# Kernel optimization log

Hardware: AMD Instinct MI355X
Metric: run time of the kernel (lower is better)

## Reference

```python
import jax, jax.numpy as jnp
import numpy as np
import math

N = 30000
E = 600000
IN_DIM = 256
HID = 64
EMB = 64
HEADS = 4
EPS = 1e-5


def _glorot(key, shape):
    fan_in, fan_out = shape[0], shape[1]
    lim = math.sqrt(6.0 / (fan_in + fan_out))
    return jax.random.uniform(key, shape, jnp.float32, -lim, lim)


def setup_inputs() -> dict:
    key = jax.random.key(0)
    ks = jax.random.split(key, 24)
    inp = {
        "x": jax.random.normal(ks[0], (N, IN_DIM), jnp.float32),
        "edge_index": jax.random.randint(ks[1], (2, E), 0, N, jnp.int64),
    }
    # layer 1: in=IN_DIM, out per head=HID, heads=HEADS -> width HID*HEADS
    w1 = HID * HEADS
    inp.update({
        "w1q": _glorot(ks[2], (IN_DIM, w1)), "b1q": jnp.zeros((w1,), jnp.float32),
        "w1k": _glorot(ks[3], (IN_DIM, w1)), "b1k": jnp.zeros((w1,), jnp.float32),
        "w1v": _glorot(ks[4], (IN_DIM, w1)), "b1v": jnp.zeros((w1,), jnp.float32),
        "w1s": _glorot(ks[5], (IN_DIM, w1)), "b1s": jnp.zeros((w1,), jnp.float32),
        "g1": jnp.ones((w1,), jnp.float32), "be1": jnp.zeros((w1,), jnp.float32),
    })
    # layer 2: in=HID*HEADS, out per head=EMB -> width EMB*HEADS
    w2 = EMB * HEADS
    inp.update({
        "w2q": _glorot(ks[6], (w1, w2)), "b2q": jnp.zeros((w2,), jnp.float32),
        "w2k": _glorot(ks[7], (w1, w2)), "b2k": jnp.zeros((w2,), jnp.float32),
        "w2v": _glorot(ks[8], (w1, w2)), "b2v": jnp.zeros((w2,), jnp.float32),
        "w2s": _glorot(ks[9], (w1, w2)), "b2s": jnp.zeros((w2,), jnp.float32),
        "g2": jnp.ones((w2,), jnp.float32), "be2": jnp.zeros((w2,), jnp.float32),
    })
    return inp


def transformer_conv(x, edge_index, wq, bq, wk, bk, wv, bv, ws, bs, heads, out_ch):
    n = x.shape[0]
    q = (x @ wq + bq).reshape(n, heads, out_ch)
    k = (x @ wk + bk).reshape(n, heads, out_ch)
    v = (x @ wv + bv).reshape(n, heads, out_ch)
    src, dst = edge_index[0], edge_index[1]
    # per-edge gather: [E, H, C]
    qi, kj, vj = q[dst], k[src], v[src]
    alpha = jnp.sum(qi * kj, axis=-1) / math.sqrt(out_ch)  # [E, H]
    # segment softmax over incoming edges of each target node
    amax = jax.lax.stop_gradient(jax.ops.segment_max(alpha, dst, num_segments=n))
    ex = jnp.exp(alpha - amax[dst])
    denom = jax.ops.segment_sum(ex, dst, num_segments=n)
    alpha = ex / denom[dst]
    # scatter-add weighted values back to targets
    out = jax.ops.segment_sum(vj * alpha[..., None], dst, num_segments=n)
    out = out.reshape(n, heads * out_ch)
    return out + x @ ws + bs  # root/skip connection


def batch_norm(x, gamma, beta):
    mean = jnp.mean(x, axis=0)
    var = jnp.mean(jnp.square(x - mean), axis=0)  # biased, training-mode BN
    return (x - mean) * jax.lax.rsqrt(var + EPS) * gamma + beta


def leaky_relu(x):
    return jnp.where(x >= 0, x, 0.1 * x)


def reference(x, edge_index, w1q, b1q, w1k, b1k, w1v, b1v, w1s, b1s, g1, be1,
              w2q, b2q, w2k, b2k, w2v, b2v, w2s, b2s, g2, be2):
    h = transformer_conv(x, edge_index, w1q, b1q, w1k, b1k, w1v, b1v, w1s, b1s, HEADS, HID)
    h = leaky_relu(batch_norm(h, g1, be1))
    h = transformer_conv(h, edge_index, w2q, b2q, w2k, b2k, w2v, b2v, w2s, b2s, HEADS, EMB)
    h = leaky_relu(batch_norm(h, g2, be2))
    return h
```

## Files before the change

kernel.cpp:

```cpp
#include <hip/hip_runtime.h>
#include <math.h>

#define NODES 30000
#define EDGES 600000
#define QKVS_W 1024
#define OUT_W 256
#define BN_EPS 1e-5f

typedef __attribute__((ext_vector_type(8))) __bf16 bf16x8;
typedef __attribute__((ext_vector_type(4))) float f32x4;

__device__ __forceinline__ unsigned short f2bf(float f) {
    union { float f; unsigned int u; } v; v.f = f;
    unsigned int r = v.u + 0x7FFFu + ((v.u >> 16) & 1u);
    return (unsigned short)(r >> 16);
}
__device__ __forceinline__ float bf2f(unsigned short u) {
    union { unsigned int u; float f; } v; v.u = ((unsigned int)u) << 16;
    return v.f;
}
__device__ __forceinline__ float bflo(unsigned int u) {
    union { unsigned int u; float f; } v; v.u = u << 16;
    return v.f;
}
__device__ __forceinline__ float bfhi(unsigned int u) {
    union { unsigned int u; float f; } v; v.u = u & 0xffff0000u;
    return v.f;
}

typedef const __attribute__((address_space(1))) void* gas_p;
typedef __attribute__((address_space(3))) void* las_p;
__device__ __forceinline__ void gload_lds16(const void* g, void* l) {
    __builtin_amdgcn_global_load_lds((gas_p)g, (las_p)l, 16, 0, 0);
}


__global__ __launch_bounds__(256) void k_count(const int* __restrict__ ei, int* __restrict__ deg) {
    int e = blockIdx.x * 256 + threadIdx.x;
    if (e < EDGES) atomicAdd(&deg[ei[EDGES + e]], 1);
}

__global__ __launch_bounds__(256) void k_blocksum(const int* __restrict__ deg, int* __restrict__ bsum) {
    __shared__ int sh[256];
    int i = blockIdx.x * 256 + threadIdx.x;
    sh[threadIdx.x] = (i < NODES) ? deg[i] : 0;
    __syncthreads();
    for (int off = 128; off > 0; off >>= 1) {
        if (threadIdx.x < off) sh[threadIdx.x] += sh[threadIdx.x + off];
        __syncthreads();
    }
    if (threadIdx.x == 0) bsum[blockIdx.x] = sh[0];
}

__global__ __launch_bounds__(128) void k_scanb(const int* __restrict__ bsum, int* __restrict__ bbase, int nb) {
    __shared__ int sh[128];
    int t = threadIdx.x;
    int v = (t < nb) ? bsum[t] : 0;
    sh[t] = v;
    __syncthreads();
    for (int off = 1; off < 128; off <<= 1) {
        int add = (t >= off) ? sh[t - off] : 0;
        __syncthreads();
        sh[t] += add;
        __syncthreads();
    }
    if (t < nb) bbase[t] = sh[t] - v;
}

__global__ __launch_bounds__(256) void k_localscan(const int* __restrict__ deg, const int* __restrict__ bbase,
                                                   int* __restrict__ rowptr, int* __restrict__ cursor) {
    __shared__ int sh[256];
    int i = blockIdx.x * 256 + threadIdx.x;
    int v = (i < NODES) ? deg[i] : 0;
    sh[threadIdx.x] = v;
    __syncthreads();
    for (int off = 1; off < 256; off <<= 1) {
        int add = (threadIdx.x >= off) ? sh[threadIdx.x - off] : 0;
        __syncthreads();
        sh[threadIdx.x] += add;
        __syncthreads();
    }
    if (i < NODES) {
        int p = bbase[blockIdx.x] + sh[threadIdx.x] - v;
        rowptr[i] = p;
        cursor[i] = p;
    }
}

__global__ __launch_bounds__(256) void k_fill(const int* __restrict__ ei, int* __restrict__ cursor,
                                              int* __restrict__ csr_src) {
    int e = blockIdx.x * 256 + threadIdx.x;
    if (e < EDGES) {
        int s = ei[e];
        int d = ei[EDGES + e];
        int slot = atomicAdd(&cursor[d], 1);
        csr_src[slot] = s;
    }
}


__global__ __launch_bounds__(256) void k_castA(const float* __restrict__ in, unsigned short* __restrict__ out, int n8) {
    int i = blockIdx.x * 256 + threadIdx.x;
    if (i >= n8) return;
    const float4* p = (const float4*)(in + (size_t)i * 8);
    float4 v0 = p[0], v1 = p[1];
    ushort4 o0, o1;
    o0.x = f2bf(v0.x); o0.y = f2bf(v0.y); o0.z = f2bf(v0.z); o0.w = f2bf(v0.w);
    o1.x = f2bf(v1.x); o1.y = f2bf(v1.y); o1.z = f2bf(v1.z); o1.w = f2bf(v1.w);
    ushort4* q = (ushort4*)(out + (size_t)i * 8);
    q[0] = o0; q[1] = o1;
}

__global__ __launch_bounds__(256) void k_castW2(
    const float* __restrict__ Wa0, const float* __restrict__ Wa1,
    const float* __restrict__ Wa2, const float* __restrict__ Wa3,
    const float* __restrict__ Ba0, const float* __restrict__ Ba1,
    const float* __restrict__ Ba2, const float* __restrict__ Ba3,
    const float* __restrict__ Wb0, const float* __restrict__ Wb1,
    const float* __restrict__ Wb2, const float* __restrict__ Wb3,
    const float* __restrict__ Bb0, const float* __restrict__ Bb1,
    const float* __restrict__ Bb2, const float* __restrict__ Bb3,
    unsigned short* __restrict__ Wt1, float* __restrict__ bf1,
    unsigned short* __restrict__ Wt2, float* __restrict__ bf2)
{
    int nn0 = blockIdx.x;
    int layer = nn0 >> 10;
    int n = nn0 & 1023;
    int k = threadIdx.x;
    int wsel = n >> 8, nc = n & 255;
    const float* W; const float* Bv;
    if (layer == 0) {
        W  = (wsel == 0) ? Wa0 : (wsel == 1) ? Wa1 : (wsel == 2) ? Wa2 : Wa3;
        Bv = (wsel == 0) ? Ba0 : (wsel == 1) ? Ba1 : (wsel == 2) ? Ba2 : Ba3;
    } else {
        W  = (wsel == 0) ? Wb0 : (wsel == 1) ? Wb1 : (wsel == 2) ? Wb2 : Wb3;
        Bv = (wsel == 0) ? Bb0 : (wsel == 1) ? Bb1 : (wsel == 2) ? Bb2 : Bb3;
    }
    unsigned short* Wt = (layer == 0) ? Wt1 : Wt2;
    float* bfused = (layer == 0) ? bf1 : bf2;
    Wt[(size_t)n * 256 + k] = f2bf(W[(size_t)k * 256 + nc]);
    if (k == 0) bfused[n] = Bv[nc];
}


#define CS 136

__global__ __launch_bounds__(256) void k_gemm_bf16(
    const unsigned short* __restrict__ A,
    const unsigned short* __restrict__ Wt,
    const float* __restrict__ bias,
    unsigned short* __restrict__ C, int M)
{
    __shared__ unsigned short sbuf[128 * CS];
    unsigned short* As = sbuf;
    unsigned short* Bs = sbuf + 8192;
    int tid = threadIdx.x;
    int lane = tid & 63;
    int wave = tid >> 6;
    int wm = wave & 1, wn = wave >> 1;
    int row0 = blockIdx.x * 128;
    int n0 = blockIdx.y * 128;

    f32x4 acc[4][4] = {};

    for (int k0 = 0; k0 < 256; k0 += 64) {
        #pragma unroll
        for (int w = 0; w < 4; w++) {
            int c = w * 256 + tid;
            int row = c >> 3;
            int cole = (c & 7) * 8;
            int ar = row0 + row; if (ar >= M) ar = M - 1;
            gload_lds16(&A[(size_t)ar * 256 + k0 + cole], &As[w * 2048 + tid * 8]);
            gload_lds16(&Wt[(size_t)(n0 + row) * 256 + k0 + cole], &Bs[w * 2048 + tid * 8]);
        }
        __syncthreads();
        int rsel = lane & 15;
        int kq = (lane >> 4) * 8;
        #pragma unroll
        for (int kh = 0; kh < 2; kh++) {
            bf16x8 af[4], bf[4];
            #pragma unroll
            for (int t = 0; t < 4; t++) {
                af[t] = *reinterpret_cast<const bf16x8*>(&As[(wm * 64 + t * 16 + rsel) * 64 + kh * 32 + kq]);
                bf[t] = *reinterpret_cast<const bf16x8*>(&Bs[(wn * 64 + t * 16 + rsel) * 64 + kh * 32 + kq]);
            }
            #pragma unroll
            for (int mt = 0; mt < 4; mt++)
                #pragma unroll
                for (int nt = 0; nt < 4; nt++)
                    acc[mt][nt] = __builtin_amdgcn_mfma_f32_16x16x32_bf16(af[mt], bf[nt], acc[mt][nt], 0, 0, 0);
        }
        __syncthreads();
    }

    int crow = (lane >> 4) * 4;
    int ccol = lane & 15;
    #pragma unroll
    for (int mt = 0; mt < 4; mt++) {
        int lrow = wm * 64 + mt * 16 + crow;
        #pragma unroll
        for (int nt = 0; nt < 4; nt++) {
            int lcol = wn * 64 + nt * 16 + ccol;
            float bv = bias[n0 + lcol];
            #pragma unroll
            for (int r = 0; r < 4; r++)
                sbuf[(lrow + r) * CS + lcol] = f2bf(acc[mt][nt][r] + bv);
        }
    }
    __syncthreads();
    int chunk = tid & 15;
    int rbase = tid >> 4;
    #pragma unroll
    for (int g = 0; g < 8; g++) {
        int row_l = g * 16 + rbase;
        int gr = row0 + row_l;
        if (gr < M) {
            uint4 val = *(const uint4*)&sbuf[row_l * CS + chunk * 8];
            *(uint4*)&C[(size_t)gr * QKVS_W + n0 + chunk * 8] = val;
        }
    }
}


__global__ __launch_bounds__(256) void k_attn_bf16(const unsigned short* __restrict__ qkvs,
                                                   const int* __restrict__ rowptr,
                                                   const int* __restrict__ deg,
                                                   const int* __restrict__ csr_src,
                                                   float* __restrict__ out)
{
    int wave = threadIdx.x >> 6;
    int lane = threadIdx.x & 63;
    int node = blockIdx.x * 4 + wave;
    if (node >= NODES) return;
    int half = lane >> 5;
    int lh = lane & 31;

    const unsigned short* qrow = qkvs + (size_t)node * QKVS_W;
    float qf0, qf1, qf2, qf3, qf4, qf5, qf6, qf7;
    {
        uint4 qv = *(const uint4*)&qrow[lh * 8];
        qf0 = bflo(qv.x); qf1 = bfhi(qv.x);
        qf2 = bflo(qv.y); qf3 = bfhi(qv.y);
        qf4 = bflo(qv.z); qf5 = bfhi(qv.z);
        qf6 = bflo(qv.w); qf7 = bfhi(qv.w);
    }

    int start = rowptr[node];
    int cnt = deg[node];
    int npairs = (cnt + 1) >> 1;

    float m = -INFINITY, L = 0.f;
    float acc[8] = {0.f, 0.f, 0.f, 0.f, 0.f, 0.f, 0.f, 0.f};

    if (cnt > 0) {
        int clast = cnt - 1;
        int e0 = 0 * 2 + half; if (e0 > clast) e0 = clast;
        int e1 = 1 * 2 + half; if (e1 > clast) e1 = clast;
        int e2 = 2 * 2 + half; if (e2 > clast) e2 = clast;
        int e3 = 3 * 2 + half; if (e3 > clast) e3 = clast;
        int ix0 = csr_src[start + e0];
        int ix1 = csr_src[start + e1];
        int ix2 = csr_src[start + e2];
        int ix3 = csr_src[start + e3];
        uint4 k0v, v0v, k1v, v1v;
        {
            const unsigned short* p = qkvs + (size_t)ix0 * QKVS_W + lh * 8;
            k0v = *(const uint4*)(p + 256);
            v0v = *(const uint4*)(p + 512);
        }
        {
            const unsigned short* p = qkvs + (size_t)ix1 * QKVS_W + lh * 8;
            k1v = *(const uint4*)(p + 256);
            v1v = *(const uint4*)(p + 512);
        }
        for (int i = 0; i < npairs; i++) {
            int en = (i + 4) * 2 + half; if (en > clast) en = clast;
            int ixn = csr_src[start + en];
            uint4 knv, vnv;
            {
                const unsigned short* p = qkvs + (size_t)ix2 * QKVS_W + lh * 8;
                knv = *(const uint4*)(p + 256);
                vnv = *(const uint4*)(p + 512);
            }
            int e = 2 * i + half;
            bool valid = e < cnt;
            float d;
            d = qf0 * bflo(k0v.x);
            d = fmaf(qf1, bfhi(k0v.x), d);
            d = fmaf(qf2, bflo(k0v.y), d);
            d = fmaf(qf3, bfhi(k0v.y), d);
            d = fmaf(qf4, bflo(k0v.z), d);
            d = fmaf(qf5, bfhi(k0v.z), d);
            d = fmaf(qf6, bflo(k0v.w), d);
            d = fmaf(qf7, bfhi(k0v.w), d);
            d += __shfl_xor(d, 1, 64);
            d += __shfl_xor(d, 2, 64);
            d += __shfl_xor(d, 4, 64);
            float al = d * 0.125f;
            if (valid) {
                if (__any(al > m + 8.f)) {
                    float nm = fmaxf(m, al);
                    float sc = __expf(m - nm);
                    L *= sc;
                    #pragma unroll
                    for (int j = 0; j < 8; j++) acc[j] *= sc;
                    m = nm;
                }
                float p = __expf(al - m);
                L += p;
                acc[0] = fmaf(p, bflo(v0v.x), acc[0]);
                acc[1] = fmaf(p, bfhi(v0v.x), acc[1]);
                acc[2] = fmaf(p, bflo(v0v.y), acc[2]);
                acc[3] = fmaf(p, bfhi(v0v.y), acc[3]);
                acc[4] = fmaf(p, bflo(v0v.z), acc[4]);
                acc[5] = fmaf(p, bfhi(v0v.z), acc[5]);
                acc[6] = fmaf(p, bflo(v0v.w), acc[6]);
                acc[7] = fmaf(p, bfhi(v0v.w), acc[7]);
            }
            k0v = k1v; v0v = v1v; k1v = knv; v1v = vnv;
            ix2 = ix3; ix3 = ixn;
        }
    }

    float mo = __shfl_xor(m, 32, 64);
    float Lo = __shfl_xor(L, 32, 64);
    float nm = fmaxf(m, mo);
    float scs = (L  > 0.f) ? __expf(m  - nm) : 0.f;
    float sco = (Lo > 0.f) ? __expf(mo - nm) : 0.f;
    float Lt = fmaf(L, scs, Lo * sco);
    float inv = (Lt > 0.f) ? 1.f / Lt : 0.f;
    float t0 = fmaf(acc[0], scs, __shfl_xor(acc[0], 32, 64) * sco);
    float t1 = fmaf(acc[1], scs, __shfl_xor(acc[1], 32, 64) * sco);
    float t2 = fmaf(acc[2], scs, __shfl_xor(acc[2], 32, 64) * sco);
    float t3 = fmaf(acc[3], scs, __shfl_xor(acc[3], 32, 64) * sco);
    float t4 = fmaf(acc[4], scs, __shfl_xor(acc[4], 32, 64) * sco);
    float t5 = fmaf(acc[5], scs, __shfl_xor(acc[5], 32, 64) * sco);
    float t6 = fmaf(acc[6], scs, __shfl_xor(acc[6], 32, 64) * sco);
    float t7 = fmaf(acc[7], scs, __shfl_xor(acc[7], 32, 64) * sco);
    float w0 = half ? t4 : t0;
    float w1 = half ? t5 : t1;
    float w2 = half ? t6 : t2;
    float w3 = half ? t7 : t3;
    ushort4 sv = *(const ushort4*)&qrow[768 + lh * 8 + half * 4];
    float4 o;
    o.x = fmaf(w0, inv, bf2f(sv.x));
    o.y = fmaf(w1, inv, bf2f(sv.y));
    o.z = fmaf(w2, inv, bf2f(sv.z));
    o.w = fmaf(w3, inv, bf2f(sv.w));
    *(float4*)&out[(size_t)node * OUT_W + lh * 8 + half * 4] = o;
}


__global__ __launch_bounds__(256) void k_bnstats(const float* __restrict__ h,
                                                 float* __restrict__ sum, float* __restrict__ sumsq) {
    int col = threadIdx.x;
    int r0 = blockIdx.x * 64;
    int r1 = min(r0 + 64, NODES);
    float s = 0.f, s2 = 0.f;
    for (int r = r0; r < r1; r++) {
        float v = h[(size_t)r * OUT_W + col];
        s += v; s2 += v * v;
    }
    atomicAdd(&sum[col], s);
    atomicAdd(&sumsq[col], s2);
}

__device__ __forceinline__ float4 bn_scale4(const float* sum, const float* sumsq,
                                            const float* g, const float* be,
                                            int col, float4* shift) {
    float4 s  = *(const float4*)&sum[col];
    float4 s2 = *(const float4*)&sumsq[col];
    float4 gv = *(const float4*)&g[col];
    float4 bv = *(const float4*)&be[col];
    const float invN = 1.0f / NODES;
    float4 sc, sh;
    float mean, var;
    mean = s.x * invN; var = fmaxf(s2.x * invN - mean * mean, 0.f);
    sc.x = gv.x * rsqrtf(var + BN_EPS); sh.x = bv.x - mean * sc.x;
    mean = s.y * invN; var = fmaxf(s2.y * invN - mean * mean, 0.f);
    sc.y = gv.y * rsqrtf(var + BN_EPS); sh.y = bv.y - mean * sc.y;
    mean = s.z * invN; var = fmaxf(s2.z * invN - mean * mean, 0.f);
    sc.z = gv.z * rsqrtf(var + BN_EPS); sh.z = bv.z - mean * sc.z;
    mean = s.w * invN; var = fmaxf(s2.w * invN - mean * mean, 0.f);
    sc.w = gv.w * rsqrtf(var + BN_EPS); sh.w = bv.w - mean * sc.w;
    *shift = sh;
    return sc;
}

__global__ __launch_bounds__(256) void k_bnapply_bf16(const float* __restrict__ h,
                                                      const float* __restrict__ sum,
                                                      const float* __restrict__ sumsq,
                                                      const float* __restrict__ g,
                                                      const float* __restrict__ be,
                                                      unsigned short* __restrict__ out) {
    int idx = blockIdx.x * 256 + threadIdx.x;
    int base = idx * 4;
    int col = base & (OUT_W - 1);
    float4 sh;
    float4 sc = bn_scale4(sum, sumsq, g, be, col, &sh);
    float4 v = *(const float4*)&h[base];
    float4 o;
    o.x = v.x * sc.x + sh.x; o.x = (o.x >= 0.f) ? o.x : 0.1f * o.x;
    o.y = v.y * sc.y + sh.y; o.y = (o.y >= 0.f) ? o.y : 0.1f * o.y;
    o.z = v.z * sc.z + sh.z; o.z = (o.z >= 0.f) ? o.z : 0.1f * o.z;
    o.w = v.w * sc.w + sh.w; o.w = (o.w >= 0.f) ? o.w : 0.1f * o.w;
    ushort4 u; u.x = f2bf(o.x); u.y = f2bf(o.y); u.z = f2bf(o.z); u.w = f2bf(o.w);
    *(ushort4*)&out[base] = u;
}

__global__ __launch_bounds__(256) void k_bnapply(const float* __restrict__ h,
                                                 const float* __restrict__ sum,
                                                 const float* __restrict__ sumsq,
                                                 const float* __restrict__ g,
                                                 const float* __restrict__ be,
                                                 float* __restrict__ out) {
    int idx = blockIdx.x * 256 + threadIdx.x;
    int base = idx * 4;
    int col = base & (OUT_W - 1);
    float4 sh;
    float4 sc = bn_scale4(sum, sumsq, g, be, col, &sh);
    float4 v = *(const float4*)&h[base];
    float4 o;
    o.x = v.x * sc.x + sh.x; o.x = (o.x >= 0.f) ? o.x : 0.1f * o.x;
    o.y = v.y * sc.y + sh.y; o.y = (o.y >= 0.f) ? o.y : 0.1f * o.y;
    o.z = v.z * sc.z + sh.z; o.z = (o.z >= 0.f) ? o.z : 0.1f * o.z;
    o.w = v.w * sc.w + sh.w; o.w = (o.w >= 0.f) ? o.w : 0.1f * o.w;
    *(float4*)&out[base] = o;
}


extern "C" void kernel_launch(void* const* d_in, const int* in_sizes, int n_in,
                              void* d_out, int out_size, void* d_ws, size_t ws_size,
                              hipStream_t stream) {
    const float* x  = (const float*)d_in[0];
    const int*   ei = (const int*)d_in[1];
    const float* w1[4] = {(const float*)d_in[2], (const float*)d_in[4], (const float*)d_in[6], (const float*)d_in[8]};
    const float* b1[4] = {(const float*)d_in[3], (const float*)d_in[5], (const float*)d_in[7], (const float*)d_in[9]};
    const float* g1  = (const float*)d_in[10];
    const float* be1 = (const float*)d_in[11];
    const float* w2[4] = {(const float*)d_in[12], (const float*)d_in[14], (const float*)d_in[16], (const float*)d_in[18]};
    const float* b2[4] = {(const float*)d_in[13], (const float*)d_in[15], (const float*)d_in[17], (const float*)d_in[19]};
    const float* g2  = (const float*)d_in[20];
    const float* be2 = (const float*)d_in[21];

    char* ws = (char*)d_ws;
    unsigned short* qkvsb  = (unsigned short*)(ws);
    float*          h1     = (float*)(ws + 61440000);
    unsigned short* abuf   = (unsigned short*)(ws + 92160000);
    unsigned short* wt1    = (unsigned short*)(ws + 107520000);
    unsigned short* wt2    = (unsigned short*)(ws + 108044288);
    float*          b1f    = (float*)(ws + 108568576);
    float*          b2f    = (float*)(ws + 108572672);
    int*            deg    = (int*)  (ws + 108576768);
    int*            rowptr = (int*)  (ws + 108696768);
    int*            cursor = (int*)  (ws + 108816768);
    int*            csr    = (int*)  (ws + 108936768);
    int*            bsum   = (int*)  (ws + 111336768);
    int*            bbase  = (int*)  (ws + 111337280);
    float*          sum1   = (float*)(ws + 111337792);
    float*          sq1    = (float*)(ws + 111338816);
    float*          sum2   = (float*)(ws + 111339840);
    float*          sq2    = (float*)(ws + 111340864);

    hipMemsetAsync(deg, 0, NODES * sizeof(int), stream);
    hipMemsetAsync(sum1, 0, 4096, stream);

    const int EB = (EDGES + 255) / 256;
    const int NB = (NODES + 255) / 256;

    k_castA<<<(NODES * 256 / 8 + 255) / 256, 256, 0, stream>>>(x, abuf, NODES * 256 / 8);
    k_castW2<<<2048, 256, 0, stream>>>(w1[0], w1[1], w1[2], w1[3], b1[0], b1[1], b1[2], b1[3],
                                       w2[0], w2[1], w2[2], w2[3], b2[0], b2[1], b2[2], b2[3],
                                       wt1, b1f, wt2, b2f);

    k_count    <<<EB, 256, 0, stream>>>(ei, deg);
    k_blocksum <<<NB, 256, 0, stream>>>(deg, bsum);
    k_scanb    <<<1, 128, 0, stream>>>(bsum, bbase, NB);
    k_localscan<<<NB, 256, 0, stream>>>(deg, bbase, rowptr, cursor);
    k_fill     <<<EB, 256, 0, stream>>>(ei, cursor, csr);

    dim3 ggrid((NODES + 127) / 128, 8);
    const int ANB = NODES / 4;
    const int APB = (NODES * OUT_W / 4) / 256;
    const int SNB = (NODES + 63) / 64;

    k_gemm_bf16  <<<ggrid, 256, 0, stream>>>(abuf, wt1, b1f, qkvsb, NODES);
    k_attn_bf16  <<<ANB, 256, 0, stream>>>(qkvsb, rowptr, deg, csr, h1);
    k_bnstats    <<<SNB, 256, 0, stream>>>(h1, sum1, sq1);
    k_bnapply_bf16<<<APB, 256, 0, stream>>>(h1, sum1, sq1, g1, be1, abuf);

    k_gemm_bf16  <<<ggrid, 256, 0, stream>>>(abuf, wt2, b2f, qkvsb, NODES);
    k_attn_bf16  <<<ANB, 256, 0, stream>>>(qkvsb, rowptr, deg, csr, h1);
    k_bnstats    <<<SNB, 256, 0, stream>>>(h1, sum2, sq2);
    k_bnapply    <<<APB, 256, 0, stream>>>(h1, sum2, sq2, g2, be2, (float*)d_out);
}
```

Baseline: 511.1 us.

## Process four nodes per wave with cross-node prefetch in attention kernel

The attention kernel now assigns four consecutive destination nodes to each wave instead of one. While finishing the current node it prefetches the next node's rowptr, degree, first CSR indices, query row and first key/value rows, so the pipeline startup latency is hidden across nodes. The grid shrinks by a factor of four, which cuts parallelism and occupancy and serializes per-wave work over nodes with uneven degrees.

```diff
diff --git a/kernel.cpp b/kernel.cpp
--- a/kernel.cpp
+++ b/kernel.cpp
@@ -230,124 +230,167 @@
 {
     int wave = threadIdx.x >> 6;
     int lane = threadIdx.x & 63;
-    int node = blockIdx.x * 4 + wave;
-    if (node >= NODES) return;
     int half = lane >> 5;
     int lh = lane & 31;
-
-    const unsigned short* qrow = qkvs + (size_t)node * QKVS_W;
-    float qf0, qf1, qf2, qf3, qf4, qf5, qf6, qf7;
+    int base = (blockIdx.x * 4 + wave) * 4;
+
+    int start = rowptr[base];
+    int cnt   = deg[base];
+    int clast = (cnt > 0) ? cnt - 1 : 0;
+    int e0 = half;     if (e0 > clast) e0 = clast;
+    int e1 = 2 + half; if (e1 > clast) e1 = clast;
+    int e2 = 4 + half; if (e2 > clast) e2 = clast;
+    int e3 = 6 + half; if (e3 > clast) e3 = clast;
+    int p0 = start + e0; if (p0 >= EDGES) p0 = EDGES - 1;
+    int p1 = start + e1; if (p1 >= EDGES) p1 = EDGES - 1;
+    int p2 = start + e2; if (p2 >= EDGES) p2 = EDGES - 1;
+    int p3 = start + e3; if (p3 >= EDGES) p3 = EDGES - 1;
+    int ix0 = csr_src[p0];
+    int ix1 = csr_src[p1];
+    int ix2 = csr_src[p2];
+    int ix3 = csr_src[p3];
+    uint4 qv = *(const uint4*)&qkvs[(size_t)base * QKVS_W + lh * 8];
+    uint4 k0v, v0v, k1v, v1v;
     {
-        uint4 qv = *(const uint4*)&qrow[lh * 8];
-        qf0 = bflo(qv.x); qf1 = bfhi(qv.x);
-        qf2 = bflo(qv.y); qf3 = bfhi(qv.y);
-        qf4 = bflo(qv.z); qf5 = bfhi(qv.z);
-        qf6 = bflo(qv.w); qf7 = bfhi(qv.w);
-    }
-
-    int start = rowptr[node];
-    int cnt = deg[node];
-    int npairs = (cnt + 1) >> 1;
-
-    float m = -INFINITY, L = 0.f;
-    float acc[8] = {0.f, 0.f, 0.f, 0.f, 0.f, 0.f, 0.f, 0.f};
-
-    if (cnt > 0) {
-        int clast = cnt - 1;
-        int e0 = 0 * 2 + half; if (e0 > clast) e0 = clast;
-        int e1 = 1 * 2 + half; if (e1 > clast) e1 = clast;
-        int e2 = 2 * 2 + half; if (e2 > clast) e2 = clast;
-        int e3 = 3 * 2 + half; if (e3 > clast) e3 = clast;
-        int ix0 = csr_src[start + e0];
-        int ix1 = csr_src[start + e1];
-        int ix2 = csr_src[start + e2];
-        int ix3 = csr_src[start + e3];
-        uint4 k0v, v0v, k1v, v1v;
-        {
-            const unsigned short* p = qkvs + (size_t)ix0 * QKVS_W + lh * 8;
-            k0v = *(const uint4*)(p + 256);
-            v0v = *(const uint4*)(p + 512);
-        }
-        {
-            const unsigned short* p = qkvs + (size_t)ix1 * QKVS_W + lh * 8;
-            k1v = *(const uint4*)(p + 256);
-            v1v = *(const uint4*)(p + 512);
-        }
-        for (int i = 0; i < npairs; i++) {
-            int en = (i + 4) * 2 + half; if (en > clast) en = clast;
-            int ixn = csr_src[start + en];
-            uint4 knv, vnv;
+        const unsigned short* p = qkvs + (size_t)ix0 * QKVS_W + lh * 8;
+        k0v = *(const uint4*)(p + 256);
+        v0v = *(const uint4*)(p + 512);
+    }
+    {
+        const unsigned short* p = qkvs + (size_t)ix1 * QKVS_W + lh * 8;
+        k1v = *(const uint4*)(p + 256);
+        v1v = *(const uint4*)(p + 512);
+    }
+
+    for (int j = 0; j < 4; j++) {
+        int node = base + j;
+        int nn = node + 1; if (nn >= NODES) nn = NODES - 1;
+        int nstart = rowptr[nn];
+        int ncnt   = deg[nn];
+
+        float qf0 = bflo(qv.x), qf1 = bfhi(qv.x);
+        float qf2 = bflo(qv.y), qf3 = bfhi(qv.y);
+        float qf4 = bflo(qv.z), qf5 = bfhi(qv.z);
+        float qf6 = bflo(qv.w), qf7 = bfhi(qv.w);
+
+        float m = -INFINITY, L = 0.f;
+        float acc[8] = {0.f, 0.f, 0.f, 0.f, 0.f, 0.f, 0.f, 0.f};
+
+        if (cnt > 0) {
+            int cl = cnt - 1;
+            int npairs = (cnt + 1) >> 1;
+            for (int i = 0; i < npairs; i++) {
+                int en = (i + 4) * 2 + half; if (en > cl) en = cl;
+                int ixn = csr_src[start + en];
+                uint4 knv, vnv;
+                {
+                    const unsigned short* p = qkvs + (size_t)ix2 * QKVS_W + lh * 8;
+                    knv = *(const uint4*)(p + 256);
+                    vnv = *(const uint4*)(p + 512);
+                }
+                int e = 2 * i + half;
+                bool valid = e < cnt;
+                float d;
+                d = qf0 * bflo(k0v.x);
+                d = fmaf(qf1, bfhi(k0v.x), d);
+                d = fmaf(qf2, bflo(k0v.y), d);
+                d = fmaf(qf3, bfhi(k0v.y), d);
+                d = fmaf(qf4, bflo(k0v.z), d);
+                d = fmaf(qf5, bfhi(k0v.z), d);
+                d = fmaf(qf6, bflo(k0v.w), d);
+                d = fmaf(qf7, bfhi(k0v.w), d);
+                d += __shfl_xor(d, 1, 64);
+                d += __shfl_xor(d, 2, 64);
+                d += __shfl_xor(d, 4, 64);
+                float al = d * 0.125f;
+                if (valid) {
+                    if (__any(al > m + 8.f)) {
+                        float nm = fmaxf(m, al);
+                        float sc = __expf(m - nm);
+                        L *= sc;
+                        #pragma unroll
+                        for (int t = 0; t < 8; t++) acc[t] *= sc;
+                        m = nm;
+                    }
+                    float p = __expf(al - m);
+                    L += p;
+                    acc[0] = fmaf(p, bflo(v0v.x), acc[0]);
+                    acc[1] = fmaf(p, bfhi(v0v.x), acc[1]);
+                    acc[2] = fmaf(p, bflo(v0v.y), acc[2]);
+                    acc[3] = fmaf(p, bfhi(v0v.y), acc[3]);
+                    acc[4] = fmaf(p, bflo(v0v.z), acc[4]);
+                    acc[5] = fmaf(p, bfhi(v0v.z), acc[5]);
+                    acc[6] = fmaf(p, bflo(v0v.w), acc[6]);
+                    acc[7] = fmaf(p, bfhi(v0v.w), acc[7]);
+                }
+                k0v = k1v; v0v = v1v; k1v = knv; v1v = vnv;
+                ix2 = ix3; ix3 = ixn;
+            }
+        }
+
+        int nix0 = 0, nix1 = 0, nix2 = 0, nix3 = 0;
+        uint4 nqv;
+        if (j < 3) {
+            int ncl = (ncnt > 0) ? ncnt - 1 : 0;
+            int f0 = half;     if (f0 > ncl) f0 = ncl;
+            int f1 = 2 + half; if (f1 > ncl) f1 = ncl;
+            int f2 = 4 + half; if (f2 > ncl) f2 = ncl;
+            int f3 = 6 + half; if (f3 > ncl) f3 = ncl;
+            int g0 = nstart + f0; if (g0 >= EDGES) g0 = EDGES - 1;
+            int g1 = nstart + f1; if (g1 >= EDGES) g1 = EDGES - 1;
+            int g2 = nstart + f2; if (g2 >= EDGES) g2 = EDGES - 1;
+            int g3 = nstart + f3; if (g3 >= EDGES) g3 = EDGES - 1;
+            nix0 = csr_src[g0];
+            nix1 = csr_src[g1];
+            nix2 = csr_src[g2];
+            nix3 = csr_src[g3];
+            nqv = *(const uint4*)&qkvs[(size_t)(node + 1) * QKVS_W + lh * 8];
+        }
+
+        const unsigned short* qrow = qkvs + (size_t)node * QKVS_W;
+        float mo = __shfl_xor(m, 32, 64);
+        float Lo = __shfl_xor(L, 32, 64);
+        float nm = fmaxf(m, mo);
+        float scs = (L  > 0.f) ? __expf(m  - nm) : 0.f;
+        float sco = (Lo > 0.f) ? __expf(mo - nm) : 0.f;
+        float Lt = fmaf(L, scs, Lo * sco);
+        float inv = (Lt > 0.f) ? 1.f / Lt : 0.f;
+        float t0 = fmaf(acc[0], scs, __shfl_xor(acc[0], 32, 64) * sco);
+        float t1 = fmaf(acc[1], scs, __shfl_xor(acc[1], 32, 64) * sco);
+        float t2 = fmaf(acc[2], scs, __shfl_xor(acc[2], 32, 64) * sco);
+        float t3 = fmaf(acc[3], scs, __shfl_xor(acc[3], 32, 64) * sco);
+        float t4 = fmaf(acc[4], scs, __shfl_xor(acc[4], 32, 64) * sco);
+        float t5 = fmaf(acc[5], scs, __shfl_xor(acc[5], 32, 64) * sco);
+        float t6 = fmaf(acc[6], scs, __shfl_xor(acc[6], 32, 64) * sco);
+        float t7 = fmaf(acc[7], scs, __shfl_xor(acc[7], 32, 64) * sco);
+        float w0 = half ? t4 : t0;
+        float w1 = half ? t5 : t1;
+        float w2 = half ? t6 : t2;
+        float w3 = half ? t7 : t3;
+        ushort4 sv = *(const ushort4*)&qrow[768 + lh * 8 + half * 4];
+        float4 o;
+        o.x = fmaf(w0, inv, bf2f(sv.x));
+        o.y = fmaf(w1, inv, bf2f(sv.y));
+        o.z = fmaf(w2, inv, bf2f(sv.z));
+        o.w = fmaf(w3, inv, bf2f(sv.w));
+        *(float4*)&out[(size_t)node * OUT_W + lh * 8 + half * 4] = o;
+
+        if (j < 3) {
             {
-                const unsigned short* p = qkvs + (size_t)ix2 * QKVS_W + lh * 8;
-                knv = *(const uint4*)(p + 256);
-                vnv = *(const uint4*)(p + 512);
+                const unsigned short* p = qkvs + (size_t)nix0 * QKVS_W + lh * 8;
+                k0v = *(const uint4*)(p + 256);
+                v0v = *(const uint4*)(p + 512);
             }
-            int e = 2 * i + half;
-            bool valid = e < cnt;
-            float d;
-            d = qf0 * bflo(k0v.x);
-            d = fmaf(qf1, bfhi(k0v.x), d);
-            d = fmaf(qf2, bflo(k0v.y), d);
-            d = fmaf(qf3, bfhi(k0v.y), d);
-            d = fmaf(qf4, bflo(k0v.z), d);
-            d = fmaf(qf5, bfhi(k0v.z), d);
-            d = fmaf(qf6, bflo(k0v.w), d);
-            d = fmaf(qf7, bfhi(k0v.w), d);
-            d += __shfl_xor(d, 1, 64);
-            d += __shfl_xor(d, 2, 64);
-            d += __shfl_xor(d, 4, 64);
-            float al = d * 0.125f;
-            if (valid) {
-                if (__any(al > m + 8.f)) {
-                    float nm = fmaxf(m, al);
-                    float sc = __expf(m - nm);
-                    L *= sc;
-                    #pragma unroll
-                    for (int j = 0; j < 8; j++) acc[j] *= sc;
-                    m = nm;
-                }
-                float p = __expf(al - m);
-                L += p;
-                acc[0] = fmaf(p, bflo(v0v.x), acc[0]);
-                acc[1] = fmaf(p, bfhi(v0v.x), acc[1]);
-                acc[2] = fmaf(p, bflo(v0v.y), acc[2]);
-                acc[3] = fmaf(p, bfhi(v0v.y), acc[3]);
-                acc[4] = fmaf(p, bflo(v0v.z), acc[4]);
-                acc[5] = fmaf(p, bfhi(v0v.z), acc[5]);
-                acc[6] = fmaf(p, bflo(v0v.w), acc[6]);
-                acc[7] = fmaf(p, bfhi(v0v.w), acc[7]);
+            {
+                const unsigned short* p = qkvs + (size_t)nix1 * QKVS_W + lh * 8;
+                k1v = *(const uint4*)(p + 256);
+                v1v = *(const uint4*)(p + 512);
             }
-            k0v = k1v; v0v = v1v; k1v = knv; v1v = vnv;
-            ix2 = ix3; ix3 = ixn;
-        }
-    }
-
-    float mo = __shfl_xor(m, 32, 64);
-    float Lo = __shfl_xor(L, 32, 64);
-    float nm = fmaxf(m, mo);
-    float scs = (L  > 0.f) ? __expf(m  - nm) : 0.f;
-    float sco = (Lo > 0.f) ? __expf(mo - nm) : 0.f;
-    float Lt = fmaf(L, scs, Lo * sco);
-    float inv = (Lt > 0.f) ? 1.f / Lt : 0.f;
-    float t0 = fmaf(acc[0], scs, __shfl_xor(acc[0], 32, 64) * sco);
-    float t1 = fmaf(acc[1], scs, __shfl_xor(acc[1], 32, 64) * sco);
-    float t2 = fmaf(acc[2], scs, __shfl_xor(acc[2], 32, 64) * sco);
-    float t3 = fmaf(acc[3], scs, __shfl_xor(acc[3], 32, 64) * sco);
-    float t4 = fmaf(acc[4], scs, __shfl_xor(acc[4], 32, 64) * sco);
-    float t5 = fmaf(acc[5], scs, __shfl_xor(acc[5], 32, 64) * sco);
-    float t6 = fmaf(acc[6], scs, __shfl_xor(acc[6], 32, 64) * sco);
-    float t7 = fmaf(acc[7], scs, __shfl_xor(acc[7], 32, 64) * sco);
-    float w0 = half ? t4 : t0;
-    float w1 = half ? t5 : t1;
-    float w2 = half ? t6 : t2;
-    float w3 = half ? t7 : t3;
-    ushort4 sv = *(const ushort4*)&qrow[768 + lh * 8 + half * 4];
-    float4 o;
-    o.x = fmaf(w0, inv, bf2f(sv.x));
-    o.y = fmaf(w1, inv, bf2f(sv.y));
-    o.z = fmaf(w2, inv, bf2f(sv.z));
-    o.w = fmaf(w3, inv, bf2f(sv.w));
-    *(float4*)&out[(size_t)node * OUT_W + lh * 8 + half * 4] = o;
+            start = nstart; cnt = ncnt;
+            ix2 = nix2; ix3 = nix3;
+            qv = nqv;
+        }
+    }
 }
 
 
@@ -480,7 +523,7 @@
     k_fill     <<<EB, 256, 0, stream>>>(ei, cursor, csr);
 
     dim3 ggrid((NODES + 127) / 128, 8);
-    const int ANB = NODES / 4;
+    const int ANB = NODES / 16;
     const int APB = (NODES * OUT_W / 4) / 256;
     const int SNB = (NODES + 63) / 64;
 
```

Result: no change. 515.7 us (+0.9%).
